# Kernel optimization log

Hardware: AMD Instinct MI355X
Metric: run time of the kernel (lower is better)

The kernel has to match this reference:

```python
import jax, jax.numpy as jnp
import numpy as np

B, N_KV, N_Q = 32, 4096, 8
D_INP, D_SLOT, HEADS, MLP_H = 256, 256, 4, 1024
ITERS = 3
EPS = 1e-8


def _ln(x, g, b, eps=1e-5):
    m = jnp.mean(x, axis=-1, keepdims=True)
    v = jnp.var(x, axis=-1, keepdims=True)
    return (x - m) * jax.lax.rsqrt(v + eps) * g + b


def setup_inputs() -> dict:
    key = jax.random.key(0)
    ks = jax.random.split(key, 12)
    def w(k, shape, fan_in):
        return jax.random.normal(k, shape, jnp.float32) / np.float32(np.sqrt(fan_in))
    return {
        "inputs": jax.random.normal(ks[0], (B, N_KV, D_INP), jnp.float32),
        "slots": jax.random.normal(ks[1], (B, N_Q, D_SLOT), jnp.float32),
        "ln_in_g": jnp.ones((D_INP,), jnp.float32), "ln_in_b": jnp.zeros((D_INP,), jnp.float32),
        "ln_slot_g": jnp.ones((D_SLOT,), jnp.float32), "ln_slot_b": jnp.zeros((D_SLOT,), jnp.float32),
        "ln_mlp_g": jnp.ones((D_SLOT,), jnp.float32), "ln_mlp_b": jnp.zeros((D_SLOT,), jnp.float32),
        "Wq": w(ks[2], (D_SLOT, D_SLOT), D_SLOT),
        "Wk": w(ks[3], (D_SLOT, D_INP), D_INP),
        "Wv": w(ks[4], (D_SLOT, D_INP), D_INP),
        "W_ih": w(ks[5], (3 * D_SLOT, D_SLOT), D_SLOT),
        "W_hh": w(ks[6], (3 * D_SLOT, D_SLOT), D_SLOT),
        "b_ih": jnp.zeros((3 * D_SLOT,), jnp.float32),
        "b_hh": jnp.zeros((3 * D_SLOT,), jnp.float32),
        "W1": w(ks[7], (MLP_H, D_SLOT), D_SLOT), "b1": jnp.zeros((MLP_H,), jnp.float32),
        "W2": w(ks[8], (D_SLOT, MLP_H), MLP_H), "b2": jnp.zeros((D_SLOT,), jnp.float32),
    }


def reference(inputs, slots, ln_in_g, ln_in_b, ln_slot_g, ln_slot_b, ln_mlp_g, ln_mlp_b,
              Wq, Wk, Wv, W_ih, W_hh, b_ih, b_hh, W1, b1, W2, b2):
    Bb, Nkv, _ = inputs.shape
    _, Nq, Ds = slots.shape
    hd = Ds // HEADS

    x = _ln(inputs, ln_in_g, ln_in_b)
    # k, v: [B, H, N_kv, hd]; k pre-scaled by hd**-0.5 as in the original
    k = (x @ Wk.T).reshape(Bb, Nkv, HEADS, hd).transpose(0, 2, 1, 3) * (hd ** -0.5)
    v = (x @ Wv.T).reshape(Bb, Nkv, HEADS, hd).transpose(0, 2, 1, 3)

    attn_vis = attn_temp = None
    for it in range(ITERS):
        if it == ITERS - 1:
            slots = jax.lax.stop_gradient(slots)
        slots_prev = slots
        s = _ln(slots, ln_slot_g, ln_slot_b)
        q = (s @ Wq.T).reshape(Bb, Nq, HEADS, hd).transpose(0, 2, 1, 3)  # [B,H,Nq,hd]
        logits = jnp.einsum('bhnd,bhqd->bhnq', k, q)  # [B,H,Nkv,Nq]
        # competing softmax: normalize jointly over (head, slot) per input token
        lt = logits.transpose(0, 2, 1, 3).reshape(Bb, Nkv, HEADS * Nq)
        attn = jax.nn.softmax(lt, axis=-1).reshape(Bb, Nkv, HEADS, Nq).transpose(0, 2, 1, 3)
        attn_vis = attn.sum(axis=1)   # [B, Nkv, Nq]
        attn_temp = attn_vis          # original recomputes the identical softmax; same values
        a = attn + EPS
        a = a / a.sum(axis=-2, keepdims=True)  # renormalize over N_kv
        updates = jnp.einsum('bhnq,bhnd->bhqd', a, v).transpose(0, 2, 1, 3).reshape(Bb, Nq, Ds)
        # GRU cell (torch GRUCell math)
        gx = updates @ W_ih.T + b_ih
        gh = slots_prev @ W_hh.T + b_hh
        xr, xz, xn = jnp.split(gx, 3, axis=-1)
        hr, hz, hn = jnp.split(gh, 3, axis=-1)
        r = jax.nn.sigmoid(xr + hr)
        z = jax.nn.sigmoid(xz + hz)
        n = jnp.tanh(xn + r * hn)
        slots = (1.0 - z) * n + z * slots_prev
        # MLP with residual
        m = _ln(slots, ln_mlp_g, ln_mlp_b)
        slots = slots + (jax.nn.relu(m @ W1.T + b1) @ W2.T + b2)
    return slots, attn_vis, attn_temp
```

## Files before the change

kernel.cpp:

```cpp
#include <hip/hip_runtime.h>
#include <math.h>


#define NKV   4096
#define DD    256
#define HQN   32
#define EPSR  1e-8f

#define WS_V      0
#define WS_A0     262144
#define WS_A1     263168
#define WS_C0     264192
#define WS_C1     265216
#define WS_SLOTA  266240
#define WS_SLOTB  331776
#define WS_WQT    397312
#define WS_WPGXH  462848
#define WS_WFT    856064
#define WS_WHHT   1249280
#define WS_W1T    1347584
#define WS_W2T    1478656
#define WS_RS     1609728
#define WS_RM     1740800
#define WS_VPART  1871872
#define WS_APART  10260480

typedef float f32x4 __attribute__((ext_vector_type(4)));
typedef short s16x8 __attribute__((ext_vector_type(8)));
typedef int   v2i   __attribute__((ext_vector_type(2)));

__device__ __forceinline__ unsigned bfr(float f) {
    unsigned u = __float_as_uint(f);
    return (u + 0x7fffu + ((u >> 16) & 1u)) >> 16;
}
__device__ __forceinline__ unsigned pk2(float lo, float hi) {
    return bfr(lo) | (bfr(hi) << 16);
}
__device__ __forceinline__ float bf2f(unsigned short us) {
    return __uint_as_float((unsigned)us << 16);
}
__device__ __forceinline__ float bflo(unsigned u) { return __uint_as_float(u << 16); }
__device__ __forceinline__ float bfhi(unsigned u) { return __uint_as_float(u & 0xffff0000u); }

__device__ __forceinline__ v2i tr_read(unsigned addr) {
    v2i d;
    asm volatile("ds_read_b64_tr_b16 %0, %1" : "=v"(d) : "v"(addr));
    return d;
}
__device__ __forceinline__ s16x8 mk_frag(v2i a, v2i b) {
    union { int i[4]; s16x8 s; } u;
    u.i[0] = a.x; u.i[1] = a.y; u.i[2] = b.x; u.i[3] = b.y;
    return u.s;
}

__global__ __launch_bounds__(256) void k_setup(
    const float* __restrict__ Wq, const float* __restrict__ Wih,
    const float* __restrict__ Wv, const float* __restrict__ Whh,
    const float* __restrict__ W1, const float* __restrict__ W2,
    float* __restrict__ wqt, unsigned* __restrict__ WfT2,
    unsigned* __restrict__ WhhT2, unsigned* __restrict__ W1T2,
    unsigned* __restrict__ W2T2)
{
    const int blk = blockIdx.x;
    const int t = threadIdx.x;
    if (blk < 64) {
        __shared__ float tile[32][33];
        int bx = (blk & 7) * 32, by = (blk >> 3) * 32;
        int tx = t & 31, ty = t >> 5;
        #pragma unroll
        for (int k = 0; k < 32; k += 8)
            tile[ty + k][tx] = Wq[(size_t)(by + ty + k) * 256 + bx + tx];
        __syncthreads();
        #pragma unroll
        for (int k = 0; k < 32; k += 8)
            wqt[(size_t)(bx + ty + k) * 256 + by + tx] = tile[tx][ty + k];
    } else if (blk < 832) {
        const int c = blk - 64;
        __shared__ float wr[256];
        wr[t] = Wih[(size_t)c * 256 + t];
        __syncthreads();
        const float2* wv2 = (const float2*)Wv;
        #pragma unroll
        for (int pp = 0; pp < 2; ++pp) {
            int P = pp * 256 + t;
            int h = P >> 7, p = P & 127;
            float f0 = 0.f, f1 = 0.f;
            #pragma unroll 8
            for (int d = 0; d < 64; ++d) {
                float a = wr[h * 64 + d];
                float2 v = wv2[(size_t)(h * 64 + d) * 128 + p];
                f0 = fmaf(a, v.x, f0); f1 = fmaf(a, v.y, f1);
            }
            WfT2[(size_t)P * 768 + c] = pk2(f0, f1);
        }
    } else if (blk < 960) {
        const int c2 = blk - 832;
        #pragma unroll
        for (int q = 0; q < 3; ++q) {
            int r = q * 256 + t;
            WhhT2[(size_t)c2 * 768 + r] = pk2(Whh[(size_t)r * 256 + 2 * c2],
                                              Whh[(size_t)r * 256 + 2 * c2 + 1]);
        }
    } else if (blk < 1088) {
        const int c2 = blk - 960;
        #pragma unroll
        for (int q = 0; q < 4; ++q) {
            int r = q * 256 + t;
            W1T2[(size_t)c2 * 1024 + r] = pk2(W1[(size_t)r * 256 + 2 * c2],
                                              W1[(size_t)r * 256 + 2 * c2 + 1]);
        }
    } else {
        const int c2 = blk - 1088;
        W2T2[(size_t)c2 * 256 + t] = pk2(W2[(size_t)t * 1024 + 2 * c2],
                                         W2[(size_t)t * 1024 + 2 * c2 + 1]);
    }
}

__global__ __launch_bounds__(256) void k_prep(
    const float* __restrict__ slots, const float* __restrict__ g_s, const float* __restrict__ b_s,
    const float* __restrict__ wqt, const float* __restrict__ Wk,
    const float* __restrict__ g_in, const float* __restrict__ b_in,
    unsigned short* __restrict__ wp_bf, float* __restrict__ c0_g, float* __restrict__ c1_g)
{
    __shared__ float s_lds[2048];
    __shared__ float qs[512];
    __shared__ float redc[4096];
    const int t = threadIdx.x;
    const int b = blockIdx.x, h = blockIdx.y;
    const int lane = t & 63, w = t >> 6;
    const float LNS = 0.125f * 1.44269504f;

    for (int r = w; r < 8; r += 4) {
        const float4 v = ((const float4*)(slots + ((size_t)b * 8 + r) * 256))[lane];
        float s0 = v.x + v.y + v.z + v.w;
        float s1 = v.x * v.x + v.y * v.y + v.z * v.z + v.w * v.w;
        #pragma unroll
        for (int o = 32; o >= 1; o >>= 1) { s0 += __shfl_xor(s0, o, 64); s1 += __shfl_xor(s1, o, 64); }
        float m = s0 * (1.f / 256.f);
        float rs = rsqrtf(s1 * (1.f / 256.f) - m * m + 1e-5f);
        float4 gg = ((const float4*)g_s)[lane];
        float4 bb = ((const float4*)b_s)[lane];
        float4 nn;
        nn.x = (v.x - m) * rs * gg.x + bb.x;
        nn.y = (v.y - m) * rs * gg.y + bb.y;
        nn.z = (v.z - m) * rs * gg.z + bb.z;
        nn.w = (v.w - m) * rs * gg.w + bb.w;
        ((float4*)(s_lds + r * 256))[lane] = nn;
    }
    __syncthreads();

    {
        const int qi0 = t >> 6, d = t & 63;
        float a0 = 0.f, a1 = 0.f;
        #pragma unroll 8
        for (int j = 0; j < 256; ++j) {
            float wv = wqt[j * 256 + h * 64 + d];
            a0 = fmaf(s_lds[qi0 * 256 + j], wv, a0);
            a1 = fmaf(s_lds[(qi0 + 4) * 256 + j], wv, a1);
        }
        qs[qi0 * 64 + d] = a0;
        qs[(qi0 + 4) * 64 + d] = a1;
    }
    __syncthreads();

    float a2[8];
    #pragma unroll
    for (int qi = 0; qi < 8; ++qi) a2[qi] = 0.f;
    #pragma unroll 4
    for (int d = 0; d < 64; ++d) {
        float wv = Wk[(size_t)(h * 64 + d) * 256 + t];
        #pragma unroll
        for (int qi = 0; qi < 8; ++qi) a2[qi] = fmaf(qs[qi * 64 + d], wv, a2[qi]);
    }
    const float gv = g_in[t], bv = b_in[t];
    #pragma unroll
    for (int qi = 0; qi < 8; ++qi) {
        float kv = LNS * a2[qi];
        float we = kv * gv;
        wp_bf[((size_t)b * HQN + h * 8 + qi) * 256 + t] = (unsigned short)bfr(we);
        redc[qi * 256 + t] = we;
        redc[2048 + qi * 256 + t] = kv * bv;
    }
    __syncthreads();
    #pragma unroll
    for (int rep = 0; rep < 2; ++rep) {
        int r = w * 2 + rep;
        float sv1 = redc[r * 256 + lane] + redc[r * 256 + 64 + lane] +
                    redc[r * 256 + 128 + lane] + redc[r * 256 + 192 + lane];
        float sv0 = redc[2048 + r * 256 + lane] + redc[2048 + r * 256 + 64 + lane] +
                    redc[2048 + r * 256 + 128 + lane] + redc[2048 + r * 256 + 192 + lane];
        #pragma unroll
        for (int o = 32; o >= 1; o >>= 1) {
            sv1 += __shfl_xor(sv1, o, 64);
            sv0 += __shfl_xor(sv0, o, 64);
        }
        if (lane == 0) {
            c1_g[b * 32 + h * 8 + r] = sv1;
            c0_g[b * 32 + h * 8 + r] = sv0;
        }
    }
}

__device__ __forceinline__ void load_x(const float* __restrict__ inp, int b, int n0,
                                       int tok_s, int seg8, float4* ld) {
    const float4* row4 = (const float4*)(inp + ((size_t)b * NKV + n0 + tok_s) * 256);
    #pragma unroll
    for (int u = 0; u < 8; ++u) ld[u] = row4[(u >> 2) * 32 + seg8 * 4 + (u & 3)];
}

__device__ __forceinline__ void pack_x(const float4* ld, char* dst, int tok_s, int seg8) {
    #pragma unroll
    for (int c = 0; c < 2; ++c) {
        int nt = seg8 + 8 * c;
        #pragma unroll
        for (int h = 0; h < 2; ++h) {
            float4 fa = ld[c * 4 + h * 2], fb = ld[c * 4 + h * 2 + 1];
            uint4 pk;
            pk.x = pk2(fa.x, fa.y); pk.y = pk2(fa.z, fa.w);
            pk.z = pk2(fb.x, fb.y); pk.w = pk2(fb.z, fb.w);
            *(uint4*)(dst + nt * 1040 + tok_s * 32 + h * 16) = pk;
        }
    }
}

__device__ __forceinline__ void calc_stats(const float4* ld, float* sb,
                                           float* __restrict__ rs_g, float* __restrict__ rm_g,
                                           int b, int n0, int tok_s, int seg8) {
    float s0 = 0.f, s1 = 0.f;
    #pragma unroll
    for (int u = 0; u < 8; ++u) {
        float4 v = ld[u];
        s0 += v.x + v.y + v.z + v.w;
        s1 = fmaf(v.x, v.x, s1); s1 = fmaf(v.y, v.y, s1);
        s1 = fmaf(v.z, v.z, s1); s1 = fmaf(v.w, v.w, s1);
    }
    s0 += __shfl_xor(s0, 1, 64); s1 += __shfl_xor(s1, 1, 64);
    s0 += __shfl_xor(s0, 2, 64); s1 += __shfl_xor(s1, 2, 64);
    s0 += __shfl_xor(s0, 4, 64); s1 += __shfl_xor(s1, 4, 64);
    float m  = s0 * (1.f / 256.f);
    float rs = rsqrtf(s1 * (1.f / 256.f) - m * m + 1e-5f);
    if (seg8 == 0) {
        sb[tok_s] = rs;
        sb[32 + tok_s] = rs * m;
        rs_g[b * 4096 + n0 + tok_s] = rs;
        rm_g[b * 4096 + n0 + tok_s] = rs * m;
    }
}

template<int NC, int STATS, int WVIS>
__global__ __launch_bounds__(256) void k_attn(
    const float* __restrict__ inp, const unsigned short* __restrict__ wp_bf,
    const float* __restrict__ c0_g, const float* __restrict__ c1_g,
    unsigned* __restrict__ vpart, float* __restrict__ apart,
    float* __restrict__ rs_g, float* __restrict__ rm_g,
    float* __restrict__ out_vis, float* __restrict__ out_temp)
{
    constexpr int KBMAX = 128 / NC;
    __shared__ unsigned short xb[8320];
    __shared__ unsigned short wl[8192];
    __shared__ unsigned short pt[1024];
    __shared__ float stats[2][64];

    const int t = threadIdx.x;
    const int l = t & 63, w = t >> 6;
    const int g = l >> 4, li = l & 15;
    const int b = blockIdx.y, kb = blockIdx.x;

    char* xbB = (char*)xb;
    char* wlB = (char*)wl;
    char* ptB = (char*)pt;
    const int tok_s = t >> 3, seg8 = t & 7;
    const int cbase = kb * NC;

    {
        const uint4* wp4 = (const uint4*)wp_bf + ((size_t)b * 8192 + (t >> 3) * 256 + (t & 7) * 32) / 8;
        const int hq = t >> 3, sg = t & 7;
        #pragma unroll
        for (int q = 0; q < 4; ++q) {
            uint4 v = wp4[q];
            *(uint4*)(wlB + hq * 512 + (((sg * 4 + q) ^ (hq & 7)) * 16)) = v;
        }
    }
// ... 94 lines not shown
                int slot = (tk >> 3) ^ ((hq >> 1) & 3);
                sv += bf2f(*(const unsigned short*)(ptB + hq * 64 + slot * 16 + (tk & 7) * 2));
            }
            float vv = sv / stats[cur][tk];
            size_t o = ((size_t)b * NKV + n0 + tk) * 8 + q;
            out_vis[o] = vv; out_temp[o] = vv;
        }

        if (ci < NC - 1) {
            if (STATS) {
                calc_stats(ldN, &stats[nxt][0], rs_g, rm_g, b, n0 + 32, tok_s, seg8);
            } else {
                if (t < 32) stats[nxt][t] = rs_g[b * 4096 + n0 + 32 + t];
                else if (t < 64) stats[nxt][t] = rm_g[b * 4096 + n0 + 32 + t - 32];
            }
        }

        {
            s16x8 pa = *(const s16x8*)(ptB + hqA * 64 + ((g ^ ((hqA >> 1) & 3)) * 16));
            unsigned abase = xbase + g * 256 + li * 8;
            v2i t0a = tr_read(abase + (ntb + 0) * 1040);
            v2i t0b = tr_read(abase + (ntb + 0) * 1040 + 128);
            v2i t1a = tr_read(abase + (ntb + 1) * 1040);
            v2i t1b = tr_read(abase + (ntb + 1) * 1040 + 128);
            v2i t2a = tr_read(abase + (ntb + 2) * 1040);
            v2i t2b = tr_read(abase + (ntb + 2) * 1040 + 128);
            v2i t3a = tr_read(abase + (ntb + 3) * 1040);
            v2i t3b = tr_read(abase + (ntb + 3) * 1040 + 128);
            asm volatile("s_waitcnt lgkmcnt(0)" ::: "memory");
            __builtin_amdgcn_sched_barrier(0);
            __builtin_amdgcn_s_setprio(1);
            av[0] = __builtin_amdgcn_mfma_f32_16x16x32_bf16(pa, mk_frag(t0a, t0b), av[0], 0, 0, 0);
            av[1] = __builtin_amdgcn_mfma_f32_16x16x32_bf16(pa, mk_frag(t1a, t1b), av[1], 0, 0, 0);
            av[2] = __builtin_amdgcn_mfma_f32_16x16x32_bf16(pa, mk_frag(t2a, t2b), av[2], 0, 0, 0);
            av[3] = __builtin_amdgcn_mfma_f32_16x16x32_bf16(pa, mk_frag(t3a, t3b), av[3], 0, 0, 0);
            __builtin_amdgcn_s_setprio(0);
            v2i t4a = tr_read(abase + (ntb + 4) * 1040);
            v2i t4b = tr_read(abase + (ntb + 4) * 1040 + 128);
            v2i t5a = tr_read(abase + (ntb + 5) * 1040);
            v2i t5b = tr_read(abase + (ntb + 5) * 1040 + 128);
            v2i t6a = tr_read(abase + (ntb + 6) * 1040);
            v2i t6b = tr_read(abase + (ntb + 6) * 1040 + 128);
            v2i t7a = tr_read(abase + (ntb + 7) * 1040);
            v2i t7b = tr_read(abase + (ntb + 7) * 1040 + 128);
            asm volatile("s_waitcnt lgkmcnt(0)" ::: "memory");
            __builtin_amdgcn_sched_barrier(0);
            __builtin_amdgcn_s_setprio(1);
            av[4] = __builtin_amdgcn_mfma_f32_16x16x32_bf16(pa, mk_frag(t4a, t4b), av[4], 0, 0, 0);
            av[5] = __builtin_amdgcn_mfma_f32_16x16x32_bf16(pa, mk_frag(t5a, t5b), av[5], 0, 0, 0);
            av[6] = __builtin_amdgcn_mfma_f32_16x16x32_bf16(pa, mk_frag(t6a, t6b), av[6], 0, 0, 0);
            av[7] = __builtin_amdgcn_mfma_f32_16x16x32_bf16(pa, mk_frag(t7a, t7b), av[7], 0, 0, 0);
            __builtin_amdgcn_s_setprio(0);
        }
        __syncthreads();

        if (ci < NC - 1) {
            pack_x(ldN, xbB, tok_s, seg8);
            __syncthreads();
        }
    }

    A0acc += __shfl_xor(A0acc, 16, 64); A0acc += __shfl_xor(A0acc, 32, 64);
    A1acc += __shfl_xor(A1acc, 16, 64); A1acc += __shfl_xor(A1acc, 32, 64);
    const size_t blk = (size_t)b * KBMAX + kb;
    if (g == 0) {
        apart[blk * 128 + Mt * 64 + hqB] = A0acc;
        apart[blk * 128 + Mt * 64 + 32 + hqB] = A1acc;
    }
    {
        #pragma unroll
        for (int r = 0; r < 4; ++r) {
            int hq = MtV * 16 + g * 4 + r;
            unsigned* vp = vpart + (blk * 32 + hq) * 128 + li;
            #pragma unroll
            for (int ip = 0; ip < 4; ++ip) {
                unsigned u = pk2(av[2 * ip][r], av[2 * ip + 1][r]);
                int jp = (ntb >> 1) + ip;
                vp[jp * 16] = u;
            }
        }
    }
}

template<int KBMAX>
__global__ __launch_bounds__(256) void k_vred(
    const unsigned* __restrict__ vpart, const float* __restrict__ apart,
    float* __restrict__ V_g, float* __restrict__ A0_g, float* __restrict__ A1_g)
{
    const int t = threadIdx.x;
    const int b = blockIdx.x;
    const int hq = blockIdx.y * 2 + (t >> 7);
    const int tl = t & 127;
    const unsigned* p = vpart + ((size_t)(b * KBMAX) * 32 + hq) * 128 + tl;
    float lo = 0.f, hi = 0.f;
    #pragma unroll 8
    for (int kb = 0; kb < KBMAX; ++kb) {
        unsigned u = p[(size_t)kb * 4096];
        lo += bflo(u); hi += bfhi(u);
    }
    const int jp = tl >> 4, li = tl & 15;
    float* vo = V_g + ((size_t)b * 32 + hq) * 256 + jp * 32 + li;
    vo[0]  = lo;
    vo[16] = hi;

    if (blockIdx.y == 0 && t < 64) {
        float s = 0.f;
        const float* ap = apart + (size_t)(b * KBMAX) * 128 + t;
        #pragma unroll 8
        for (int kb = 0; kb < KBMAX; ++kb)
            s += ap[(size_t)kb * 128] + ap[(size_t)kb * 128 + 64];
        if (t < 32) A0_g[b * 32 + t] = s;
        else        A1_g[b * 32 + t - 32] = s;
    }
}

__global__ __launch_bounds__(256) void k_gates(
    const float* __restrict__ V_g, const float* __restrict__ A0_g,
    const float* __restrict__ A1_g,
    const float* __restrict__ g_in, const float* __restrict__ b_in,
    const float* __restrict__ slot_cur,
    const unsigned* __restrict__ WfT2, const unsigned* __restrict__ WhhT2,
    float* __restrict__ gxh, float* __restrict__ slot_nxt)
{
    __shared__ __align__(16) float aT[1024 * 4];
    const int t = threadIdx.x;
    const int rg = blockIdx.y;
    const int chunk = blockIdx.x;
    const int row0 = rg * 4;
    float acc0 = 0.f, acc1 = 0.f, acc2 = 0.f, acc3 = 0.f;

    if (chunk == 0) {
        #pragma unroll
        for (int rr = 0; rr < 4; ++rr)
            slot_nxt[(size_t)(row0 + rr) * 256 + t] = 0.f;
    }

    if (chunk < 3) {
        const int b = rg >> 1, qi0 = (rg & 1) * 4;
        const float gt = g_in[t], bt = b_in[t];
        #pragma unroll
        for (int kk = 0; kk < 4; ++kk) {
            float4 y4;
            #pragma unroll
            for (int rr = 0; rr < 4; ++rr) {
                int hq = kk * 8 + qi0 + rr;
                float A0 = A0_g[b * 32 + hq], A1 = A1_g[b * 32 + hq];
                float den = A0 + EPSR * (float)NKV;
                float vv = V_g[((size_t)b * 32 + hq) * 256 + t];
                float yv = (gt * (vv - A1) + bt * A0) / den;
                ((float*)&y4)[rr] = yv;
            }
            *(float4*)(aT + (kk * 256 + t) * 4) = y4;
        }
        __syncthreads();
        const unsigned* wp = WfT2 + chunk * 256 + t;
        #pragma unroll 4
        for (int k2 = 0; k2 < 512; ++k2) {
            unsigned wv = wp[(size_t)k2 * 768];
            float w0 = bflo(wv), w1 = bfhi(wv);
            float4 a0 = *(const float4*)(aT + 8 * k2);
            float4 a1 = *(const float4*)(aT + 8 * k2 + 4);
            acc0 = fmaf(a0.x, w0, acc0); acc0 = fmaf(a1.x, w1, acc0);
            acc1 = fmaf(a0.y, w0, acc1); acc1 = fmaf(a1.y, w1, acc1);
            acc2 = fmaf(a0.z, w0, acc2); acc2 = fmaf(a1.z, w1, acc2);
            acc3 = fmaf(a0.w, w0, acc3); acc3 = fmaf(a1.w, w1, acc3);
        }
        float* go = gxh + (size_t)row0 * 1536 + chunk * 256 + t;
        go[0] = acc0; go[1536] = acc1; go[3072] = acc2; go[4608] = acc3;
    } else {
        const int gc = chunk - 3;
        {
            float4 y4;
            #pragma unroll
            for (int rr = 0; rr < 4; ++rr)
                ((float*)&y4)[rr] = slot_cur[(size_t)(row0 + rr) * 256 + t];
            *(float4*)(aT + t * 4) = y4;
        }
        __syncthreads();
        const unsigned* wp = WhhT2 + gc * 256 + t;
        #pragma unroll 4
        for (int k2 = 0; k2 < 128; ++k2) {
            unsigned wv = wp[(size_t)k2 * 768];
            float w0 = bflo(wv), w1 = bfhi(wv);
            float4 a0 = *(const float4*)(aT + 8 * k2);
            float4 a1 = *(const float4*)(aT + 8 * k2 + 4);
            acc0 = fmaf(a0.x, w0, acc0); acc0 = fmaf(a1.x, w1, acc0);
            acc1 = fmaf(a0.y, w0, acc1); acc1 = fmaf(a1.y, w1, acc1);
            acc2 = fmaf(a0.z, w0, acc2); acc2 = fmaf(a1.z, w1, acc2);
            acc3 = fmaf(a0.w, w0, acc3); acc3 = fmaf(a1.w, w1, acc3);
        }
        float* go = gxh + (size_t)row0 * 1536 + 768 + gc * 256 + t;
        go[0] = acc0; go[1536] = acc1; go[3072] = acc2; go[4608] = acc3;
    }
}

__global__ __launch_bounds__(256) void k_mlp(
    const float* __restrict__ gxh, const float* __restrict__ slot_cur,
    const float* __restrict__ bih, const float* __restrict__ bhh,
    const float* __restrict__ gm, const float* __restrict__ bm,
    const unsigned* __restrict__ W1T2, const float* __restrict__ b1,
    const unsigned* __restrict__ W2T2, const float* __restrict__ b2,
    float* __restrict__ slot_nxt)
{
    __shared__ __align__(16) float mT[1024];
    __shared__ float sm_l[4][256];
    __shared__ float h1_l[4][256];
    __shared__ float lnst[8];
    const int t = threadIdx.x;
    const int rg = blockIdx.y, chunk = blockIdx.x;
    const int row0 = rg * 4;
    const int lane = t & 63, w = t >> 6;

    const float bi0 = bih[t], bi1 = bih[256 + t], bi2 = bih[512 + t];
    const float bh0 = bhh[t], bh1 = bhh[256 + t], bh2 = bhh[512 + t];
    float smid[4];
    #pragma unroll
    for (int rr = 0; rr < 4; ++rr) {
        const float* gr = gxh + (size_t)(row0 + rr) * 1536;
        float gx0 = gr[t], gx1 = gr[256 + t], gx2 = gr[512 + t];
        float gh0 = gr[768 + t], gh1 = gr[1024 + t], gh2 = gr[1280 + t];
        float spv = slot_cur[(size_t)(row0 + rr) * 256 + t];
        float r = 1.f / (1.f + __expf(-(gx0 + bi0 + gh0 + bh0)));
        float z = 1.f / (1.f + __expf(-(gx1 + bi1 + gh1 + bh1)));
        float n = tanhf(gx2 + bi2 + r * (gh2 + bh2));
        smid[rr] = (1.f - z) * n + z * spv;
        sm_l[rr][t] = smid[rr];
    }
    __syncthreads();
    {
        float4 v = *(const float4*)(&sm_l[w][lane * 4]);
        float s0 = v.x + v.y + v.z + v.w;
        float s1 = v.x * v.x + v.y * v.y + v.z * v.z + v.w * v.w;
        #pragma unroll
        for (int o = 32; o >= 1; o >>= 1) { s0 += __shfl_xor(s0, o, 64); s1 += __shfl_xor(s1, o, 64); }
        if (lane == 0) {
            float mu = s0 * (1.f / 256.f);
            lnst[w * 2] = mu;
            lnst[w * 2 + 1] = rsqrtf(s1 * (1.f / 256.f) - mu * mu + 1e-5f);
        }
    }
    __syncthreads();
    {
        const float gmt = gm[t], bmt = bm[t];
        float4 m4;
        #pragma unroll
        for (int rr = 0; rr < 4; ++rr)
            ((float*)&m4)[rr] = (smid[rr] - lnst[rr * 2]) * lnst[rr * 2 + 1] * gmt + bmt;
        *(float4*)(mT + t * 4) = m4;
    }
    __syncthreads();

    {
        float acc0 = 0.f, acc1 = 0.f, acc2 = 0.f, acc3 = 0.f;
        const unsigned* wp = W1T2 + chunk * 256 + t;
        #pragma unroll 4
        for (int k2 = 0; k2 < 128; ++k2) {
            unsigned wv = wp[(size_t)k2 * 1024];
            float w0 = bflo(wv), w1 = bfhi(wv);
            float4 a0 = *(const float4*)(mT + 8 * k2);
            float4 a1 = *(const float4*)(mT + 8 * k2 + 4);
            acc0 = fmaf(a0.x, w0, acc0); acc0 = fmaf(a1.x, w1, acc0);
            acc1 = fmaf(a0.y, w0, acc1); acc1 = fmaf(a1.y, w1, acc1);
            acc2 = fmaf(a0.z, w0, acc2); acc2 = fmaf(a1.z, w1, acc2);
            acc3 = fmaf(a0.w, w0, acc3); acc3 = fmaf(a1.w, w1, acc3);
        }
        const float b1t = b1[chunk * 256 + t];
        h1_l[0][t] = fmaxf(acc0 + b1t, 0.f);
        h1_l[1][t] = fmaxf(acc1 + b1t, 0.f);
        h1_l[2][t] = fmaxf(acc2 + b1t, 0.f);
        h1_l[3][t] = fmaxf(acc3 + b1t, 0.f);
    }
    __syncthreads();

    {
        float o0 = 0.f, o1 = 0.f, o2 = 0.f, o3 = 0.f;
        const unsigned* wp = W2T2 + (size_t)(chunk * 128) * 256 + t;
        #pragma unroll 4
        for (int k2 = 0; k2 < 128; ++k2) {
            unsigned wv = wp[(size_t)k2 * 256];
            float w0 = bflo(wv), w1 = bfhi(wv);
            float a00 = h1_l[0][2 * k2], a01 = h1_l[0][2 * k2 + 1];
            float a10 = h1_l[1][2 * k2], a11 = h1_l[1][2 * k2 + 1];
            float a20 = h1_l[2][2 * k2], a21 = h1_l[2][2 * k2 + 1];
            float a30 = h1_l[3][2 * k2], a31 = h1_l[3][2 * k2 + 1];
            o0 = fmaf(a00, w0, o0); o0 = fmaf(a01, w1, o0);
            o1 = fmaf(a10, w0, o1); o1 = fmaf(a11, w1, o1);
            o2 = fmaf(a20, w0, o2); o2 = fmaf(a21, w1, o2);
            o3 = fmaf(a30, w0, o3); o3 = fmaf(a31, w1, o3);
        }
        const float b2t = b2[t];
        float p0 = o0 + ((chunk == 0) ? smid[0] + b2t : 0.f);
        float p1 = o1 + ((chunk == 0) ? smid[1] + b2t : 0.f);
        float p2 = o2 + ((chunk == 0) ? smid[2] + b2t : 0.f);
        float p3 = o3 + ((chunk == 0) ? smid[3] + b2t : 0.f);
        atomicAdd(slot_nxt + (size_t)(row0 + 0) * 256 + t, p0);
        atomicAdd(slot_nxt + (size_t)(row0 + 1) * 256 + t, p1);
        atomicAdd(slot_nxt + (size_t)(row0 + 2) * 256 + t, p2);
        atomicAdd(slot_nxt + (size_t)(row0 + 3) * 256 + t, p3);
    }
}

extern "C" void kernel_launch(void* const* d_in, const int* in_sizes, int n_in,
                              void* d_out, int out_size, void* d_ws, size_t ws_size,
                              hipStream_t stream) {
    const float* inp     = (const float*)d_in[0];
    const float* slots0  = (const float*)d_in[1];
    const float* ln_in_g = (const float*)d_in[2];
    const float* ln_in_b = (const float*)d_in[3];
    const float* ln_s_g  = (const float*)d_in[4];
    const float* ln_s_b  = (const float*)d_in[5];
    const float* ln_m_g  = (const float*)d_in[6];
    const float* ln_m_b  = (const float*)d_in[7];
    const float* Wq  = (const float*)d_in[8];
    const float* Wk  = (const float*)d_in[9];
    const float* Wv  = (const float*)d_in[10];
    const float* Wih = (const float*)d_in[11];
    const float* Whh = (const float*)d_in[12];
    const float* bih = (const float*)d_in[13];
    const float* bhh = (const float*)d_in[14];
    const float* W1  = (const float*)d_in[15];
    const float* b1  = (const float*)d_in[16];
    const float* W2  = (const float*)d_in[17];
    const float* b2  = (const float*)d_in[18];

    float* ws = (float*)d_ws;
    float* V_g   = ws + WS_V;
    float* A0_g  = ws + WS_A0;
    float* A1_g  = ws + WS_A1;
    float* c0_g  = ws + WS_C0;
    float* c1_g  = ws + WS_C1;
    float* slotA = ws + WS_SLOTA;
    float* slotB = ws + WS_SLOTB;
    float* wqt   = ws + WS_WQT;
    float* gxh   = ws + WS_WPGXH;
    unsigned short* wp_bf = (unsigned short*)(ws + WS_WPGXH);
    unsigned* WfT2  = (unsigned*)(ws + WS_WFT);
    unsigned* WhhT2 = (unsigned*)(ws + WS_WHHT);
    unsigned* W1T2  = (unsigned*)(ws + WS_W1T);
    unsigned* W2T2  = (unsigned*)(ws + WS_W2T);
    float* rs_g  = ws + WS_RS;
    float* rm_g  = ws + WS_RM;
    unsigned* vpart = (unsigned*)(ws + WS_VPART);
    float* apart = ws + WS_APART;

    float* out_slots = (float*)d_out;
    float* out_vis   = out_slots + 32 * 8 * 256;
    float* out_temp  = out_vis + 32 * 4096 * 8;

    k_setup<<<1600, 256, 0, stream>>>(Wq, Wih, Wv, Whh, W1, W2,
                                      wqt, WfT2, WhhT2, W1T2, W2T2);

    for (int it = 0; it < 3; ++it) {
        const float* cur = (it == 0) ? slots0 : ((it == 1) ? slotB : slotA);
        float* nxt = (it == 0) ? slotB : ((it == 1) ? slotA : out_slots);
        k_prep<<<dim3(32, 4), 256, 0, stream>>>(cur, ln_s_g, ln_s_b, wqt, Wk,
                                                ln_in_g, ln_in_b, wp_bf, c0_g, c1_g);
        if (it == 0)
            k_attn<2, 1, 0><<<dim3(64, 32), 256, 0, stream>>>(
                inp, wp_bf, c0_g, c1_g, vpart, apart, rs_g, rm_g, out_vis, out_temp);
        else if (it == 1)
            k_attn<2, 0, 0><<<dim3(64, 32), 256, 0, stream>>>(
                inp, wp_bf, c0_g, c1_g, vpart, apart, rs_g, rm_g, out_vis, out_temp);
        else
            k_attn<2, 0, 1><<<dim3(64, 32), 256, 0, stream>>>(
                inp, wp_bf, c0_g, c1_g, vpart, apart, rs_g, rm_g, out_vis, out_temp);
        k_vred<64><<<dim3(32, 16), 256, 0, stream>>>(vpart, apart, V_g, A0_g, A1_g);
        k_gates<<<dim3(6, 64), 256, 0, stream>>>(
            V_g, A0_g, A1_g, ln_in_g, ln_in_b, cur, WfT2, WhhT2, gxh, nxt);
        k_mlp<<<dim3(4, 64), 256, 0, stream>>>(
            gxh, cur, bih, bhh, ln_m_g, ln_m_b, W1T2, b1, W2T2, b2, nxt);
    }
}
```

Baseline: 430.0 us.

## Fuse vred, gates, MLP and next-iteration prep into one cooperative kernel

```diff
diff --git a/kernel.cpp b/kernel.cpp
--- a/kernel.cpp
+++ b/kernel.cpp
@@ -1,5 +1,8 @@
 #include <hip/hip_runtime.h>
+#include <hip/hip_cooperative_groups.h>
 #include <math.h>
+
+namespace cg = cooperative_groups;
 
 
 #define NKV   4096
@@ -116,17 +119,16 @@
     }
 }
 
-__global__ __launch_bounds__(256) void k_prep(
+
+__device__ void prep_body(float* sh, int b, int h, int t,
     const float* __restrict__ slots, const float* __restrict__ g_s, const float* __restrict__ b_s,
     const float* __restrict__ wqt, const float* __restrict__ Wk,
     const float* __restrict__ g_in, const float* __restrict__ b_in,
     unsigned short* __restrict__ wp_bf, float* __restrict__ c0_g, float* __restrict__ c1_g)
 {
-    __shared__ float s_lds[2048];
-    __shared__ float qs[512];
-    __shared__ float redc[4096];
-    const int t = threadIdx.x;
-    const int b = blockIdx.x, h = blockIdx.y;
+    float* s_lds = sh;
+    float* qs    = sh + 2048;
+    float* redc  = sh + 2560;
     const int lane = t & 63, w = t >> 6;
     const float LNS = 0.125f * 1.44269504f;
 
@@ -198,6 +200,300 @@
             c1_g[b * 32 + h * 8 + r] = sv1;
             c0_g[b * 32 + h * 8 + r] = sv0;
         }
+    }
+}
+
+template<int KBMAX>
+__device__ void vred_body(int b, int y, int t,
+    const unsigned* __restrict__ vpart, const float* __restrict__ apart,
+    float* __restrict__ V_g, float* __restrict__ A0_g, float* __restrict__ A1_g)
+{
+    const int hq = y * 2 + (t >> 7);
+    const int tl = t & 127;
+    const unsigned* p = vpart + ((size_t)(b * KBMAX) * 32 + hq) * 128 + tl;
+    float lo = 0.f, hi = 0.f;
+    #pragma unroll 8
+    for (int kb = 0; kb < KBMAX; ++kb) {
+        unsigned u = p[(size_t)kb * 4096];
+        lo += bflo(u); hi += bfhi(u);
+    }
+    const int jp = tl >> 4, li = tl & 15;
+    float* vo = V_g + ((size_t)b * 32 + hq) * 256 + jp * 32 + li;
+    vo[0]  = lo;
+    vo[16] = hi;
+
+    if (y == 0 && t < 64) {
+        float s = 0.f;
+        const float* ap = apart + (size_t)(b * KBMAX) * 128 + t;
+        #pragma unroll 8
+        for (int kb = 0; kb < KBMAX; ++kb)
+            s += ap[(size_t)kb * 128] + ap[(size_t)kb * 128 + 64];
+        if (t < 32) A0_g[b * 32 + t] = s;
+        else        A1_g[b * 32 + t - 32] = s;
+    }
+}
+
+__device__ void gates_body(float* sh, int chunk, int rg, int t,
+    const float* __restrict__ V_g, const float* __restrict__ A0_g,
+    const float* __restrict__ A1_g,
+    const float* __restrict__ g_in, const float* __restrict__ b_in,
+    const float* __restrict__ slot_cur,
+    const unsigned* __restrict__ WfT2, const unsigned* __restrict__ WhhT2,
+    float* __restrict__ gxh, float* __restrict__ slot_nxt)
+{
+    float* aT = sh;
+    const int row0 = rg * 4;
+    float acc0 = 0.f, acc1 = 0.f, acc2 = 0.f, acc3 = 0.f;
+
+    if (chunk == 0) {
+        #pragma unroll
+        for (int rr = 0; rr < 4; ++rr)
+            slot_nxt[(size_t)(row0 + rr) * 256 + t] = 0.f;
+    }
+
+    if (chunk < 3) {
+        const int b = rg >> 1, qi0 = (rg & 1) * 4;
+        const float gt = g_in[t], bt = b_in[t];
+        #pragma unroll
+        for (int kk = 0; kk < 4; ++kk) {
+            float4 y4;
+            #pragma unroll
+            for (int rr = 0; rr < 4; ++rr) {
+                int hq = kk * 8 + qi0 + rr;
+                float A0 = A0_g[b * 32 + hq], A1 = A1_g[b * 32 + hq];
+                float den = A0 + EPSR * (float)NKV;
+                float vv = V_g[((size_t)b * 32 + hq) * 256 + t];
+                float yv = (gt * (vv - A1) + bt * A0) / den;
+                ((float*)&y4)[rr] = yv;
+            }
+            *(float4*)(aT + (kk * 256 + t) * 4) = y4;
+        }
+        __syncthreads();
+        const unsigned* wp = WfT2 + chunk * 256 + t;
+        #pragma unroll 4
+        for (int k2 = 0; k2 < 512; ++k2) {
+            unsigned wv = wp[(size_t)k2 * 768];
+            float w0 = bflo(wv), w1 = bfhi(wv);
+            float4 a0 = *(const float4*)(aT + 8 * k2);
+            float4 a1 = *(const float4*)(aT + 8 * k2 + 4);
+            acc0 = fmaf(a0.x, w0, acc0); acc0 = fmaf(a1.x, w1, acc0);
+            acc1 = fmaf(a0.y, w0, acc1); acc1 = fmaf(a1.y, w1, acc1);
+            acc2 = fmaf(a0.z, w0, acc2); acc2 = fmaf(a1.z, w1, acc2);
+            acc3 = fmaf(a0.w, w0, acc3); acc3 = fmaf(a1.w, w1, acc3);
+        }
+        float* go = gxh + (size_t)row0 * 1536 + chunk * 256 + t;
+        go[0] = acc0; go[1536] = acc1; go[3072] = acc2; go[4608] = acc3;
+    } else {
+        const int gc = chunk - 3;
+        {
+            float4 y4;
+            #pragma unroll
+            for (int rr = 0; rr < 4; ++rr)
+                ((float*)&y4)[rr] = slot_cur[(size_t)(row0 + rr) * 256 + t];
+            *(float4*)(aT + t * 4) = y4;
+        }
+        __syncthreads();
+        const unsigned* wp = WhhT2 + gc * 256 + t;
+        #pragma unroll 4
+        for (int k2 = 0; k2 < 128; ++k2) {
+            unsigned wv = wp[(size_t)k2 * 768];
+            float w0 = bflo(wv), w1 = bfhi(wv);
+            float4 a0 = *(const float4*)(aT + 8 * k2);
+            float4 a1 = *(const float4*)(aT + 8 * k2 + 4);
+            acc0 = fmaf(a0.x, w0, acc0); acc0 = fmaf(a1.x, w1, acc0);
+            acc1 = fmaf(a0.y, w0, acc1); acc1 = fmaf(a1.y, w1, acc1);
+            acc2 = fmaf(a0.z, w0, acc2); acc2 = fmaf(a1.z, w1, acc2);
+            acc3 = fmaf(a0.w, w0, acc3); acc3 = fmaf(a1.w, w1, acc3);
+        }
+        float* go = gxh + (size_t)row0 * 1536 + 768 + gc * 256 + t;
+        go[0] = acc0; go[1536] = acc1; go[3072] = acc2; go[4608] = acc3;
+    }
+}
+
+__device__ void mlp_body(float* sh, int chunk, int rg, int t,
+    const float* __restrict__ gxh, const float* __restrict__ slot_cur,
+    const float* __restrict__ bih, const float* __restrict__ bhh,
+    const float* __restrict__ gm, const float* __restrict__ bm,
+    const unsigned* __restrict__ W1T2, const float* __restrict__ b1,
+    const unsigned* __restrict__ W2T2, const float* __restrict__ b2,
+    float* __restrict__ slot_nxt)
+{
+    float* mT   = sh;
+    float* sm   = sh + 1024;
+    float* h1   = sh + 2048;
+    float* lnst = sh + 3072;
+    const int row0 = rg * 4;
+    const int lane = t & 63, w = t >> 6;
+
+    const float bi0 = bih[t], bi1 = bih[256 + t], bi2 = bih[512 + t];
+    const float bh0 = bhh[t], bh1 = bhh[256 + t], bh2 = bhh[512 + t];
+    float smid[4];
+    #pragma unroll
+    for (int rr = 0; rr < 4; ++rr) {
+        const float* gr = gxh + (size_t)(row0 + rr) * 1536;
+        float gx0 = gr[t], gx1 = gr[256 + t], gx2 = gr[512 + t];
+        float gh0 = gr[768 + t], gh1 = gr[1024 + t], gh2 = gr[1280 + t];
+        float spv = slot_cur[(size_t)(row0 + rr) * 256 + t];
+        float r = 1.f / (1.f + __expf(-(gx0 + bi0 + gh0 + bh0)));
+        float z = 1.f / (1.f + __expf(-(gx1 + bi1 + gh1 + bh1)));
+        float n = tanhf(gx2 + bi2 + r * (gh2 + bh2));
+        smid[rr] = (1.f - z) * n + z * spv;
+        sm[rr * 256 + t] = smid[rr];
+    }
+    __syncthreads();
+    {
+        float4 v = *(const float4*)(&sm[w * 256 + lane * 4]);
+        float s0 = v.x + v.y + v.z + v.w;
+        float s1 = v.x * v.x + v.y * v.y + v.z * v.z + v.w * v.w;
+        #pragma unroll
+        for (int o = 32; o >= 1; o >>= 1) { s0 += __shfl_xor(s0, o, 64); s1 += __shfl_xor(s1, o, 64); }
+        if (lane == 0) {
+            float mu = s0 * (1.f / 256.f);
+            lnst[w * 2] = mu;
+            lnst[w * 2 + 1] = rsqrtf(s1 * (1.f / 256.f) - mu * mu + 1e-5f);
+        }
+    }
+    __syncthreads();
+    {
+        const float gmt = gm[t], bmt = bm[t];
+        float4 m4;
+        #pragma unroll
+        for (int rr = 0; rr < 4; ++rr)
+            ((float*)&m4)[rr] = (smid[rr] - lnst[rr * 2]) * lnst[rr * 2 + 1] * gmt + bmt;
+        *(float4*)(mT + t * 4) = m4;
+    }
+    __syncthreads();
+
+    {
+        float acc0 = 0.f, acc1 = 0.f, acc2 = 0.f, acc3 = 0.f;
+        const unsigned* wp = W1T2 + chunk * 256 + t;
+        #pragma unroll 4
+        for (int k2 = 0; k2 < 128; ++k2) {
+            unsigned wv = wp[(size_t)k2 * 1024];
+            float w0 = bflo(wv), w1 = bfhi(wv);
+            float4 a0 = *(const float4*)(mT + 8 * k2);
+            float4 a1 = *(const float4*)(mT + 8 * k2 + 4);
+            acc0 = fmaf(a0.x, w0, acc0); acc0 = fmaf(a1.x, w1, acc0);
+            acc1 = fmaf(a0.y, w0, acc1); acc1 = fmaf(a1.y, w1, acc1);
+            acc2 = fmaf(a0.z, w0, acc2); acc2 = fmaf(a1.z, w1, acc2);
+            acc3 = fmaf(a0.w, w0, acc3); acc3 = fmaf(a1.w, w1, acc3);
+        }
+        const float b1t = b1[chunk * 256 + t];
+        h1[0 * 256 + t] = fmaxf(acc0 + b1t, 0.f);
+        h1[1 * 256 + t] = fmaxf(acc1 + b1t, 0.f);
+        h1[2 * 256 + t] = fmaxf(acc2 + b1t, 0.f);
+        h1[3 * 256 + t] = fmaxf(acc3 + b1t, 0.f);
+    }
+    __syncthreads();
+
+    {
+        float o0 = 0.f, o1 = 0.f, o2 = 0.f, o3 = 0.f;
+        const unsigned* wp = W2T2 + (size_t)(chunk * 128) * 256 + t;
+        #pragma unroll 4
+        for (int k2 = 0; k2 < 128; ++k2) {
+            unsigned wv = wp[(size_t)k2 * 256];
+            float w0 = bflo(wv), w1 = bfhi(wv);
+            float a00 = h1[2 * k2], a01 = h1[2 * k2 + 1];
+            float a10 = h1[256 + 2 * k2], a11 = h1[256 + 2 * k2 + 1];
+            float a20 = h1[512 + 2 * k2], a21 = h1[512 + 2 * k2 + 1];
+            float a30 = h1[768 + 2 * k2], a31 = h1[768 + 2 * k2 + 1];
+            o0 = fmaf(a00, w0, o0); o0 = fmaf(a01, w1, o0);
+            o1 = fmaf(a10, w0, o1); o1 = fmaf(a11, w1, o1);
+            o2 = fmaf(a20, w0, o2); o2 = fmaf(a21, w1, o2);
+            o3 = fmaf(a30, w0, o3); o3 = fmaf(a31, w1, o3);
+        }
+        const float b2t = b2[t];
+        float p0 = o0 + ((chunk == 0) ? smid[0] + b2t : 0.f);
+        float p1 = o1 + ((chunk == 0) ? smid[1] + b2t : 0.f);
+        float p2 = o2 + ((chunk == 0) ? smid[2] + b2t : 0.f);
+        float p3 = o3 + ((chunk == 0) ? smid[3] + b2t : 0.f);
+        atomicAdd(slot_nxt + (size_t)(row0 + 0) * 256 + t, p0);
+        atomicAdd(slot_nxt + (size_t)(row0 + 1) * 256 + t, p1);
+        atomicAdd(slot_nxt + (size_t)(row0 + 2) * 256 + t, p2);
+        atomicAdd(slot_nxt + (size_t)(row0 + 3) * 256 + t, p3);
+    }
+}
+
+__global__ __launch_bounds__(256) void k_prep(
+    const float* slots, const float* g_s, const float* b_s,
+    const float* wqt, const float* Wk, const float* g_in, const float* b_in,
+    unsigned short* wp_bf, float* c0_g, float* c1_g)
+{
+    __shared__ __align__(16) float sh[6656];
+    prep_body(sh, blockIdx.x, blockIdx.y, threadIdx.x,
+              slots, g_s, b_s, wqt, Wk, g_in, b_in, wp_bf, c0_g, c1_g);
+}
+
+__global__ __launch_bounds__(256) void k_vred(
+    const unsigned* vpart, const float* apart,
+    float* V_g, float* A0_g, float* A1_g)
+{
+    vred_body<64>(blockIdx.x, blockIdx.y, threadIdx.x, vpart, apart, V_g, A0_g, A1_g);
+}
+
+__global__ __launch_bounds__(256) void k_gates(
+    const float* V_g, const float* A0_g, const float* A1_g,
+    const float* g_in, const float* b_in, const float* slot_cur,
+    const unsigned* WfT2, const unsigned* WhhT2,
+    float* gxh, float* slot_nxt)
+{
+    __shared__ __align__(16) float sh[4096];
+    gates_body(sh, blockIdx.x, blockIdx.y, threadIdx.x,
+               V_g, A0_g, A1_g, g_in, b_in, slot_cur, WfT2, WhhT2, gxh, slot_nxt);
+}
+
+__global__ __launch_bounds__(256) void k_mlp(
+    const float* gxh, const float* slot_cur,
+    const float* bih, const float* bhh, const float* gm, const float* bm,
+    const unsigned* W1T2, const float* b1, const unsigned* W2T2, const float* b2,
+    float* slot_nxt)
+{
+    __shared__ __align__(16) float sh[3080];
+    mlp_body(sh, blockIdx.x, blockIdx.y, threadIdx.x,
+             gxh, slot_cur, bih, bhh, gm, bm, W1T2, b1, W2T2, b2, slot_nxt);
+}
+
+__global__ __launch_bounds__(256) void k_tail(
+    const unsigned* vpart, const float* apart,
+    float* V_g, float* A0_g, float* A1_g,
+    const float* g_in, const float* b_in,
+    const float* slot_cur,
+    const unsigned* WfT2, const unsigned* WhhT2,
+    float* gxh, float* slot_nxt,
+    const float* bih, const float* bhh,
+    const float* gm, const float* bm,
+    const unsigned* W1T2, const float* b1,
+    const unsigned* W2T2, const float* b2,
+    const float* g_s, const float* b_s,
+    const float* wqt, const float* Wk,
+    unsigned short* wp_bf, float* c0_g, float* c1_g,
+    int do_prep)
+{
+    cg::grid_group grid = cg::this_grid();
+    __shared__ __align__(16) float sh[6656];
+    const int blk = blockIdx.x;
+    const int t = threadIdx.x;
+
+    vred_body<64>(blk >> 4, blk & 15, t, vpart, apart, V_g, A0_g, A1_g);
+    __threadfence();
+    grid.sync();
+
+    if (blk < 384)
+        gates_body(sh, blk % 6, blk / 6, t, V_g, A0_g, A1_g,
+                   g_in, b_in, slot_cur, WfT2, WhhT2, gxh, slot_nxt);
+    __threadfence();
+    grid.sync();
+
+    if (blk < 256)
+        mlp_body(sh, blk & 3, blk >> 2, t, gxh, slot_cur,
+                 bih, bhh, gm, bm, W1T2, b1, W2T2, b2, slot_nxt);
+
+    if (do_prep) {
+        __threadfence();
+        grid.sync();
+        if (blk < 128)
+            prep_body(sh, blk >> 2, blk & 3, t, slot_nxt, g_s, b_s,
+                      wqt, Wk, g_in, b_in, wp_bf, c0_g, c1_g);
     }
 }
 
@@ -458,224 +754,6 @@
     }
 }
 
-template<int KBMAX>
-__global__ __launch_bounds__(256) void k_vred(
-    const unsigned* __restrict__ vpart, const float* __restrict__ apart,
-    float* __restrict__ V_g, float* __restrict__ A0_g, float* __restrict__ A1_g)
-{
-    const int t = threadIdx.x;
-    const int b = blockIdx.x;
-    const int hq = blockIdx.y * 2 + (t >> 7);
-    const int tl = t & 127;
-    const unsigned* p = vpart + ((size_t)(b * KBMAX) * 32 + hq) * 128 + tl;
-    float lo = 0.f, hi = 0.f;
-    #pragma unroll 8
-    for (int kb = 0; kb < KBMAX; ++kb) {
-        unsigned u = p[(size_t)kb * 4096];
-        lo += bflo(u); hi += bfhi(u);
-    }
-    const int jp = tl >> 4, li = tl & 15;
-    float* vo = V_g + ((size_t)b * 32 + hq) * 256 + jp * 32 + li;
-    vo[0]  = lo;
-    vo[16] = hi;
-
-    if (blockIdx.y == 0 && t < 64) {
-        float s = 0.f;
-        const float* ap = apart + (size_t)(b * KBMAX) * 128 + t;
-        #pragma unroll 8
-        for (int kb = 0; kb < KBMAX; ++kb)
-            s += ap[(size_t)kb * 128] + ap[(size_t)kb * 128 + 64];
-        if (t < 32) A0_g[b * 32 + t] = s;
-        else        A1_g[b * 32 + t - 32] = s;
-    }
-}
-
-__global__ __launch_bounds__(256) void k_gates(
-    const float* __restrict__ V_g, const float* __restrict__ A0_g,
-    const float* __restrict__ A1_g,
-    const float* __restrict__ g_in, const float* __restrict__ b_in,
-    const float* __restrict__ slot_cur,
-    const unsigned* __restrict__ WfT2, const unsigned* __restrict__ WhhT2,
-    float* __restrict__ gxh, float* __restrict__ slot_nxt)
-{
-    __shared__ __align__(16) float aT[1024 * 4];
-    const int t = threadIdx.x;
-    const int rg = blockIdx.y;
-    const int chunk = blockIdx.x;
-    const int row0 = rg * 4;
-    float acc0 = 0.f, acc1 = 0.f, acc2 = 0.f, acc3 = 0.f;
-
-    if (chunk == 0) {
-        #pragma unroll
-        for (int rr = 0; rr < 4; ++rr)
-            slot_nxt[(size_t)(row0 + rr) * 256 + t] = 0.f;
-    }
-
-    if (chunk < 3) {
-        const int b = rg >> 1, qi0 = (rg & 1) * 4;
-        const float gt = g_in[t], bt = b_in[t];
-        #pragma unroll
-        for (int kk = 0; kk < 4; ++kk) {
-            float4 y4;
-            #pragma unroll
-            for (int rr = 0; rr < 4; ++rr) {
-                int hq = kk * 8 + qi0 + rr;
-                float A0 = A0_g[b * 32 + hq], A1 = A1_g[b * 32 + hq];
-                float den = A0 + EPSR * (float)NKV;
-                float vv = V_g[((size_t)b * 32 + hq) * 256 + t];
-                float yv = (gt * (vv - A1) + bt * A0) / den;
-                ((float*)&y4)[rr] = yv;
-            }
-            *(float4*)(aT + (kk * 256 + t) * 4) = y4;
-        }
-        __syncthreads();
-        const unsigned* wp = WfT2 + chunk * 256 + t;
-        #pragma unroll 4
-        for (int k2 = 0; k2 < 512; ++k2) {
-            unsigned wv = wp[(size_t)k2 * 768];
-            float w0 = bflo(wv), w1 = bfhi(wv);
-            float4 a0 = *(const float4*)(aT + 8 * k2);
-            float4 a1 = *(const float4*)(aT + 8 * k2 + 4);
-            acc0 = fmaf(a0.x, w0, acc0); acc0 = fmaf(a1.x, w1, acc0);
-            acc1 = fmaf(a0.y, w0, acc1); acc1 = fmaf(a1.y, w1, acc1);
-            acc2 = fmaf(a0.z, w0, acc2); acc2 = fmaf(a1.z, w1, acc2);
-            acc3 = fmaf(a0.w, w0, acc3); acc3 = fmaf(a1.w, w1, acc3);
-        }
-        float* go = gxh + (size_t)row0 * 1536 + chunk * 256 + t;
-        go[0] = acc0; go[1536] = acc1; go[3072] = acc2; go[4608] = acc3;
-    } else {
-        const int gc = chunk - 3;
-        {
-            float4 y4;
-            #pragma unroll
-            for (int rr = 0; rr < 4; ++rr)
-                ((float*)&y4)[rr] = slot_cur[(size_t)(row0 + rr) * 256 + t];
-            *(float4*)(aT + t * 4) = y4;
-        }
-        __syncthreads();
-        const unsigned* wp = WhhT2 + gc * 256 + t;
-        #pragma unroll 4
-        for (int k2 = 0; k2 < 128; ++k2) {
-            unsigned wv = wp[(size_t)k2 * 768];
-            float w0 = bflo(wv), w1 = bfhi(wv);
-            float4 a0 = *(const float4*)(aT + 8 * k2);
-            float4 a1 = *(const float4*)(aT + 8 * k2 + 4);
-            acc0 = fmaf(a0.x, w0, acc0); acc0 = fmaf(a1.x, w1, acc0);
-            acc1 = fmaf(a0.y, w0, acc1); acc1 = fmaf(a1.y, w1, acc1);
-            acc2 = fmaf(a0.z, w0, acc2); acc2 = fmaf(a1.z, w1, acc2);
-            acc3 = fmaf(a0.w, w0, acc3); acc3 = fmaf(a1.w, w1, acc3);
-        }
-        float* go = gxh + (size_t)row0 * 1536 + 768 + gc * 256 + t;
-        go[0] = acc0; go[1536] = acc1; go[3072] = acc2; go[4608] = acc3;
-    }
-}
-
-__global__ __launch_bounds__(256) void k_mlp(
-    const float* __restrict__ gxh, const float* __restrict__ slot_cur,
-    const float* __restrict__ bih, const float* __restrict__ bhh,
-    const float* __restrict__ gm, const float* __restrict__ bm,
-    const unsigned* __restrict__ W1T2, const float* __restrict__ b1,
-    const unsigned* __restrict__ W2T2, const float* __restrict__ b2,
-    float* __restrict__ slot_nxt)
-{
-    __shared__ __align__(16) float mT[1024];
-    __shared__ float sm_l[4][256];
-    __shared__ float h1_l[4][256];
-    __shared__ float lnst[8];
-    const int t = threadIdx.x;
-    const int rg = blockIdx.y, chunk = blockIdx.x;
-    const int row0 = rg * 4;
-    const int lane = t & 63, w = t >> 6;
-
-    const float bi0 = bih[t], bi1 = bih[256 + t], bi2 = bih[512 + t];
-    const float bh0 = bhh[t], bh1 = bhh[256 + t], bh2 = bhh[512 + t];
-    float smid[4];
-    #pragma unroll
-    for (int rr = 0; rr < 4; ++rr) {
-        const float* gr = gxh + (size_t)(row0 + rr) * 1536;
-        float gx0 = gr[t], gx1 = gr[256 + t], gx2 = gr[512 + t];
-        float gh0 = gr[768 + t], gh1 = gr[1024 + t], gh2 = gr[1280 + t];
-        float spv = slot_cur[(size_t)(row0 + rr) * 256 + t];
-        float r = 1.f / (1.f + __expf(-(gx0 + bi0 + gh0 + bh0)));
-        float z = 1.f / (1.f + __expf(-(gx1 + bi1 + gh1 + bh1)));
-        float n = tanhf(gx2 + bi2 + r * (gh2 + bh2));
-        smid[rr] = (1.f - z) * n + z * spv;
-        sm_l[rr][t] = smid[rr];
-    }
-    __syncthreads();
-    {
-        float4 v = *(const float4*)(&sm_l[w][lane * 4]);
-        float s0 = v.x + v.y + v.z + v.w;
-        float s1 = v.x * v.x + v.y * v.y + v.z * v.z + v.w * v.w;
-        #pragma unroll
-        for (int o = 32; o >= 1; o >>= 1) { s0 += __shfl_xor(s0, o, 64); s1 += __shfl_xor(s1, o, 64); }
-        if (lane == 0) {
-            float mu = s0 * (1.f / 256.f);
-            lnst[w * 2] = mu;
-            lnst[w * 2 + 1] = rsqrtf(s1 * (1.f / 256.f) - mu * mu + 1e-5f);
-        }
-    }
-    __syncthreads();
-    {
-        const float gmt = gm[t], bmt = bm[t];
-        float4 m4;
-        #pragma unroll
-        for (int rr = 0; rr < 4; ++rr)
-            ((float*)&m4)[rr] = (smid[rr] - lnst[rr * 2]) * lnst[rr * 2 + 1] * gmt + bmt;
-        *(float4*)(mT + t * 4) = m4;
-    }
-    __syncthreads();
-
-    {
-        float acc0 = 0.f, acc1 = 0.f, acc2 = 0.f, acc3 = 0.f;
-        const unsigned* wp = W1T2 + chunk * 256 + t;
-        #pragma unroll 4
-        for (int k2 = 0; k2 < 128; ++k2) {
-            unsigned wv = wp[(size_t)k2 * 1024];
-            float w0 = bflo(wv), w1 = bfhi(wv);
-            float4 a0 = *(const float4*)(mT + 8 * k2);
-            float4 a1 = *(const float4*)(mT + 8 * k2 + 4);
-            acc0 = fmaf(a0.x, w0, acc0); acc0 = fmaf(a1.x, w1, acc0);
-            acc1 = fmaf(a0.y, w0, acc1); acc1 = fmaf(a1.y, w1, acc1);
-            acc2 = fmaf(a0.z, w0, acc2); acc2 = fmaf(a1.z, w1, acc2);
-            acc3 = fmaf(a0.w, w0, acc3); acc3 = fmaf(a1.w, w1, acc3);
-        }
-        const float b1t = b1[chunk * 256 + t];
-        h1_l[0][t] = fmaxf(acc0 + b1t, 0.f);
-        h1_l[1][t] = fmaxf(acc1 + b1t, 0.f);
-        h1_l[2][t] = fmaxf(acc2 + b1t, 0.f);
-        h1_l[3][t] = fmaxf(acc3 + b1t, 0.f);
-    }
-    __syncthreads();
-
-    {
-        float o0 = 0.f, o1 = 0.f, o2 = 0.f, o3 = 0.f;
-        const unsigned* wp = W2T2 + (size_t)(chunk * 128) * 256 + t;
-        #pragma unroll 4
-        for (int k2 = 0; k2 < 128; ++k2) {
-            unsigned wv = wp[(size_t)k2 * 256];
-            float w0 = bflo(wv), w1 = bfhi(wv);
-            float a00 = h1_l[0][2 * k2], a01 = h1_l[0][2 * k2 + 1];
-            float a10 = h1_l[1][2 * k2], a11 = h1_l[1][2 * k2 + 1];
-            float a20 = h1_l[2][2 * k2], a21 = h1_l[2][2 * k2 + 1];
-            float a30 = h1_l[3][2 * k2], a31 = h1_l[3][2 * k2 + 1];
-            o0 = fmaf(a00, w0, o0); o0 = fmaf(a01, w1, o0);
-            o1 = fmaf(a10, w0, o1); o1 = fmaf(a11, w1, o1);
-            o2 = fmaf(a20, w0, o2); o2 = fmaf(a21, w1, o2);
-            o3 = fmaf(a30, w0, o3); o3 = fmaf(a31, w1, o3);
-        }
-        const float b2t = b2[t];
-        float p0 = o0 + ((chunk == 0) ? smid[0] + b2t : 0.f);
-        float p1 = o1 + ((chunk == 0) ? smid[1] + b2t : 0.f);
-        float p2 = o2 + ((chunk == 0) ? smid[2] + b2t : 0.f);
-        float p3 = o3 + ((chunk == 0) ? smid[3] + b2t : 0.f);
-        atomicAdd(slot_nxt + (size_t)(row0 + 0) * 256 + t, p0);
-        atomicAdd(slot_nxt + (size_t)(row0 + 1) * 256 + t, p1);
-        atomicAdd(slot_nxt + (size_t)(row0 + 2) * 256 + t, p2);
-        atomicAdd(slot_nxt + (size_t)(row0 + 3) * 256 + t, p3);
-    }
-}
-
 extern "C" void kernel_launch(void* const* d_in, const int* in_sizes, int n_in,
                               void* d_out, int out_size, void* d_ws, size_t ws_size,
                               hipStream_t stream) {
@@ -725,12 +803,12 @@
 
     k_setup<<<1600, 256, 0, stream>>>(Wq, Wih, Wv, Whh, W1, W2,
                                       wqt, WfT2, WhhT2, W1T2, W2T2);
+    k_prep<<<dim3(32, 4), 256, 0, stream>>>(slots0, ln_s_g, ln_s_b, wqt, Wk,
+                                            ln_in_g, ln_in_b, wp_bf, c0_g, c1_g);
 
     for (int it = 0; it < 3; ++it) {
         const float* cur = (it == 0) ? slots0 : ((it == 1) ? slotB : slotA);
         float* nxt = (it == 0) ? slotB : ((it == 1) ? slotA : out_slots);
-        k_prep<<<dim3(32, 4), 256, 0, stream>>>(cur, ln_s_g, ln_s_b, wqt, Wk,
-                                                ln_in_g, ln_in_b, wp_bf, c0_g, c1_g);
         if (it == 0)
             k_attn<2, 1, 0><<<dim3(64, 32), 256, 0, stream>>>(
                 inp, wp_bf, c0_g, c1_g, vpart, apart, rs_g, rm_g, out_vis, out_temp);
@@ -740,10 +818,30 @@
         else
             k_attn<2, 0, 1><<<dim3(64, 32), 256, 0, stream>>>(
                 inp, wp_bf, c0_g, c1_g, vpart, apart, rs_g, rm_g, out_vis, out_temp);
-        k_vred<64><<<dim3(32, 16), 256, 0, stream>>>(vpart, apart, V_g, A0_g, A1_g);
-        k_gates<<<dim3(6, 64), 256, 0, stream>>>(
-            V_g, A0_g, A1_g, ln_in_g, ln_in_b, cur, WfT2, WhhT2, gxh, nxt);
-        k_mlp<<<dim3(4, 64), 256, 0, stream>>>(
-            gxh, cur, bih, bhh, ln_m_g, ln_m_b, W1T2, b1, W2T2, b2, nxt);
-    }
-}
+
+        int do_prep = (it < 2) ? 1 : 0;
+        const unsigned* vpart_c = vpart;
+        const float* apart_c = apart;
+        void* args[] = {
+            (void*)&vpart_c, (void*)&apart_c, (void*)&V_g, (void*)&A0_g, (void*)&A1_g,
+            (void*)&ln_in_g, (void*)&ln_in_b, (void*)&cur,
+            (void*)&WfT2, (void*)&WhhT2, (void*)&gxh, (void*)&nxt,
+            (void*)&bih, (void*)&bhh, (void*)&ln_m_g, (void*)&ln_m_b,
+            (void*)&W1T2, (void*)&b1, (void*)&W2T2, (void*)&b2,
+            (void*)&ln_s_g, (void*)&ln_s_b, (void*)&wqt, (void*)&Wk,
+            (void*)&wp_bf, (void*)&c0_g, (void*)&c1_g, (void*)&do_prep
+        };
+        hipError_t rc = hipLaunchCooperativeKernel(
+            (const void*)k_tail, dim3(512), dim3(256), args, 0, stream);
+        if (rc != hipSuccess) {
+            k_vred<<<dim3(32, 16), 256, 0, stream>>>(vpart, apart, V_g, A0_g, A1_g);
+            k_gates<<<dim3(6, 64), 256, 0, stream>>>(
+                V_g, A0_g, A1_g, ln_in_g, ln_in_b, cur, WfT2, WhhT2, gxh, nxt);
+            k_mlp<<<dim3(4, 64), 256, 0, stream>>>(
+                gxh, cur, bih, bhh, ln_m_g, ln_m_b, W1T2, b1, W2T2, b2, nxt);
+            if (do_prep)
+                k_prep<<<dim3(32, 4), 256, 0, stream>>>(nxt, ln_s_g, ln_s_b, wqt, Wk,
+                                                        ln_in_g, ln_in_b, wp_bf, c0_g, c1_g);
+        }
+    }
+}
```

After: 1.276 ms. +196.8%, slower.
